# Kernel tuning notes

Measured on AMD Instinct MI355X. Metric: run time of the kernel, lower is better.

Reference implementation:

```python
import jax, jax.numpy as jnp
import numpy as np

B, N, Th, Td, Tw, Tp = 8, 3000, 24, 12, 24, 12
T2a, T2b, K = 64, 32, 3  # hidden temporal dims of the two STBlocks, Cheb order


def _laplacian(A):
    # PyG ChebConv with lambda_max=None -> lambda_max=2.0, sym normalization:
    # L_hat = 2L/lambda_max - I = -D^{-1/2} A D^{-1/2} with zero diagonal
    Aod = A * (1.0 - jnp.eye(A.shape[0], dtype=A.dtype))
    deg = Aod.sum(axis=1)
    dinv = jnp.where(deg > 0, deg ** -0.5, 0.0)
    return -(dinv[:, None] * Aod * dinv[None, :])


def _cheb(x, L, W, b):
    # Chebyshev graph conv, K=3. x: (B,N,Cin), L: (N,N), W: (K,Cin,Cout), b: (Cout,)
    Tx0 = x
    Tx1 = jnp.einsum('nm,bmi->bni', L, Tx0)
    Tx2 = 2.0 * jnp.einsum('nm,bmi->bni', L, Tx1) - Tx0
    out = (jnp.einsum('bni,io->bno', Tx0, W[0])
           + jnp.einsum('bni,io->bno', Tx1, W[1])
           + jnp.einsum('bni,io->bno', Tx2, W[2]))
    return out + b


def _tconv(x, w, b):
    # Conv1d(1, 1, 3, padding=1) over last axis. x: (B,N,T), w: (3,), b: scalar
    xp = jnp.pad(x, ((0, 0), (0, 0), (1, 1)))
    return w[0] * xp[..., :-2] + w[1] * xp[..., 1:-1] + w[2] * xp[..., 2:] + b


def _stblock(x, L, W, bg, cw, cb):
    x = jax.nn.relu(_cheb(x, L, W, bg))
    return jax.nn.relu(_tconv(x, cw, cb))


def _branch(X, L, W1, b1, c1w, c1b, W2, b2, c2w, c2b, WD, bD):
    x = X.reshape(X.shape[0], X.shape[1], X.shape[3])  # (B,N,T)
    x = _stblock(x, L, W1, b1, c1w, c1b)  # (B,N,64)
    x = _stblock(x, L, W2, b2, c2w, c2b)  # (B,N,32)
    return jax.nn.relu(x @ WD + bD)       # (B,N,Tp); forward only uses LinearD


def setup_inputs() -> dict:
    ks = jax.random.split(jax.random.key(0), 48)
    it = iter(range(48))

    def nrm(shape, s=1.0):
        return jax.random.normal(ks[next(it)], shape, jnp.float32) * s

    Xh = nrm((B, N, 1, Th))
    Xd = nrm((B, N, 1, Td))
    Xw = nrm((B, N, 1, Tw))
    u = jax.random.uniform(ks[next(it)], (N, N))
    w = jax.random.uniform(ks[next(it)], (N, N))
    A = jnp.where(u < 0.01, w, 0.0)
    A = 0.5 * (A + A.T)

    def gcn_p(ti, to):
        return nrm((K, ti, to), (2.0 / (ti + to)) ** 0.5), jnp.zeros((to,), jnp.float32)

    def conv_p():
        return nrm((K,), 0.4), nrm((), 0.1)

    Wh1, bh1 = gcn_p(Th, T2a); ch1w, ch1b = conv_p()
    Wh2, bh2 = gcn_p(T2a, T2b); ch2w, ch2b = conv_p()
    Wd1, bd1 = gcn_p(Td, T2a); cd1w, cd1b = conv_p()
    Wd2, bd2 = gcn_p(T2a, T2b); cd2w, cd2b = conv_p()
    Ww1, bw1 = gcn_p(Tw, T2a); cw1w, cw1b = conv_p()
    Ww2, bw2 = gcn_p(T2a, T2b); cw2w, cw2b = conv_p()
    WD = nrm((T2b, Tp), (2.0 / (T2b + Tp)) ** 0.5)
    bD = jnp.zeros((Tp,), jnp.float32)
    Fh = jax.random.uniform(ks[next(it)], (Tp,), jnp.float32)
    Fd = jax.random.uniform(ks[next(it)], (Tp,), jnp.float32)
    Fw = jax.random.uniform(ks[next(it)], (Tp,), jnp.float32)

    return dict(Xh=Xh, Xd=Xd, Xw=Xw, A=A,
                Wh1=Wh1, bh1=bh1, ch1w=ch1w, ch1b=ch1b, Wh2=Wh2, bh2=bh2, ch2w=ch2w, ch2b=ch2b,
                Wd1=Wd1, bd1=bd1, cd1w=cd1w, cd1b=cd1b, Wd2=Wd2, bd2=bd2, cd2w=cd2w, cd2b=cd2b,
                Ww1=Ww1, bw1=bw1, cw1w=cw1w, cw1b=cw1b, Ww2=Ww2, bw2=bw2, cw2w=cw2w, cw2b=cw2b,
                WD=WD, bD=bD, Fh=Fh, Fd=Fd, Fw=Fw)


def reference(Xh, Xd, Xw, A,
              Wh1, bh1, ch1w, ch1b, Wh2, bh2, ch2w, ch2b,
              Wd1, bd1, cd1w, cd1b, Wd2, bd2, cd2w, cd2b,
              Ww1, bw1, cw1w, cw1b, Ww2, bw2, cw2w, cw2b,
              WD, bD, Fh, Fd, Fw):
    L = _laplacian(A)
    Yh = _branch(Xh, L, Wh1, bh1, ch1w, ch1b, Wh2, bh2, ch2w, ch2b, WD, bD)
    Yd = _branch(Xd, L, Wd1, bd1, cd1w, cd1b, Wd2, bd2, cd2w, cd2b, WD, bD)
    Yw = _branch(Xw, L, Ww1, bw1, cw1w, cw1b, Ww2, bw2, cw2w, cw2b, WD, bD)
    Y = Fh * Yh + Fd * Yd + Fw * Yw  # Fusion: elementwise weighted sum over Tp
    return Y[:, :, None, :]  # (B,N,1,Tp)
```

## Files before the change

### kernel.cpp

```cpp
#include <hip/hip_runtime.h>

#define NN 3000
#define NB 8
#define TP 12
#define DMAX 128
#define F1T 480
#define F2T 768
#define Z1T 1536

struct BrW {
    const float *W1[3]; const float *b1[3]; const float *c1w[3]; const float *c1b[3];
    const float *W2[3]; const float *b2[3]; const float *c2w[3]; const float *c2b[3];
    const float *Fb[3];
};

__global__ void build_kernel(const float* __restrict__ A, int* __restrict__ colp,
                             float* __restrict__ valp, int* __restrict__ cnt,
                             float* __restrict__ dinv) {
    int n = blockIdx.x;
    int lane = threadIdx.x;
    const float* row = A + (size_t)n * NN;
    int base = 0;
    float s = 0.f;
    for (int start = 0; start < NN; start += 64) {
        int m = start + lane;
        float a = 0.f; bool nz = false;
        if (m < NN && m != n) {
            a = row[m];
            nz = (a != 0.f);
        }
        s += a;
        unsigned long long mask = __ballot(nz);
        int off = __popcll(mask & ((1ull << lane) - 1ull));
        if (nz) {
            int idx = base + off;
            if (idx < DMAX) { colp[n * DMAX + idx] = m; valp[n * DMAX + idx] = a; }
        }
        base += __popcll(mask);
    }
    for (int o = 32; o > 0; o >>= 1) s += __shfl_down(s, o);
    if (lane == 0) {
        cnt[n] = (base < DMAX) ? base : DMAX;
        dinv[n] = (s > 0.f) ? 1.0f / sqrtf(s) : 0.f;
    }
}

__global__ void scale_kernel(const int* __restrict__ colp, float* __restrict__ valp,
                             const int* __restrict__ cnt, const float* __restrict__ dinv) {
    int n = blockIdx.x;
    int j = threadIdx.x;
    if (j < cnt[n]) {
        int m = colp[n * DMAX + j];
        valp[n * DMAX + j] *= -dinv[n] * dinv[m];
    }
}

__global__ void pack_kernel(const float* __restrict__ Xh, const float* __restrict__ Xd,
                            const float* __restrict__ Xw, float* __restrict__ xcat) {
    int idx = blockIdx.x * blockDim.x + threadIdx.x;
    if (idx >= NN * F1T) return;
    int n = idx / F1T, r = idx % F1T;
    const float* src; int b, t, T;
    if (r < 192)      { src = Xh; T = 24; int rr = r;       b = rr / 24; t = rr % 24; }
    else if (r < 288) { src = Xd; T = 12; int rr = r - 192; b = rr / 12; t = rr % 12; }
    else              { src = Xw; T = 24; int rr = r - 288; b = rr / 24; t = rr % 24; }
    xcat[idx] = src[((size_t)b * NN + n) * T + t];
}

template <int F, int SLICE, int EPI>
__global__ void spmm_kernel(const int* __restrict__ colp, const float* __restrict__ valp,
                            const int* __restrict__ cnt, const float* __restrict__ x,
                            const float* __restrict__ aux, float* __restrict__ y) {
    int nwg = gridDim.x;
    int q = nwg >> 3;
    int bid = blockIdx.x;
    int w = (bid & 7) * q + (bid >> 3);
    int slice = w / NN;
    int n = w - slice * NN;
    int f = slice * SLICE + threadIdx.x;

    __shared__ int   scol[DMAX];
    __shared__ float sval[DMAX];
    int c = cnt[n];
    if (threadIdx.x < DMAX) {
        int j = threadIdx.x;
        bool ok = j < c;
        scol[j] = ok ? colp[n * DMAX + j] * F : 0;
        sval[j] = ok ? valp[n * DMAX + j] : 0.f;
    }
    __syncthreads();
    int c16 = (c + 15) & ~15;
    float a0 = 0.f, a1 = 0.f, a2 = 0.f, a3 = 0.f;
    float a4 = 0.f, a5 = 0.f, a6 = 0.f, a7 = 0.f;
    if (f < F) {
        for (int i = 0; i < c16; i += 16) {
            float g[16], w16[16];
            #pragma unroll
            for (int u = 0; u < 16; ++u) {
                int cc = scol[i + u];
                w16[u] = sval[i + u];
                g[u] = x[cc + f];
            }
            a0 += w16[0] * g[0];   a1 += w16[1] * g[1];
            a2 += w16[2] * g[2];   a3 += w16[3] * g[3];
            a4 += w16[4] * g[4];   a5 += w16[5] * g[5];
            a6 += w16[6] * g[6];   a7 += w16[7] * g[7];
            a0 += w16[8] * g[8];   a1 += w16[9] * g[9];
            a2 += w16[10] * g[10]; a3 += w16[11] * g[11];
            a4 += w16[12] * g[12]; a5 += w16[13] * g[13];
            a6 += w16[14] * g[14]; a7 += w16[15] * g[15];
        }
    }
    if (f >= F) return;
    float acc = ((a0 + a1) + (a2 + a3)) + ((a4 + a5) + (a6 + a7));
    size_t o = (size_t)n * F + f;
    if (EPI == 1) acc = 2.f * acc - aux[o];
    else if (EPI == 2) acc = aux[o] + 2.f * acc;
    y[o] = acc;
}

template <int T, int OFF, int BROFF>
__device__ __forceinline__ void combine1_body(
        int unit, const float* __restrict__ xcat, const float* __restrict__ t1cat,
        const float* __restrict__ t2cat, float* __restrict__ z1cat,
        const float* __restrict__ W, const float* __restrict__ bg,
        const float* __restrict__ cw, const float* __restrict__ cb, int co) {
    int n = unit / NB, b = unit % NB;
    size_t rowbase = (size_t)n * F1T + OFF + b * T;
    float xv0 = 0.f, xv1 = 0.f, xv2 = 0.f;
    if (co < T) {
        xv0 = xcat[rowbase + co];
        xv1 = t1cat[rowbase + co];
        xv2 = t2cat[rowbase + co];
    }
    float acc = bg[co];
    #pragma unroll
    for (int i = 0; i < T; ++i)
        acc += __shfl(xv0, i) * W[i * 64 + co];
    #pragma unroll
    for (int i = 0; i < T; ++i)
        acc += __shfl(xv1, i) * W[(T + i) * 64 + co];
    #pragma unroll
    for (int i = 0; i < T; ++i)
        acc += __shfl(xv2, i) * W[(2 * T + i) * 64 + co];
    float z = fmaxf(acc, 0.f);
    float left  = __shfl_up(z, 1);
    float right = __shfl_down(z, 1);
    if (co == 0) left = 0.f;
    if (co == 63) right = 0.f;
    float w0 = cw[0], w1 = cw[1], w2 = cw[2], bb = cb[0];
    float o = fmaxf(w0 * left + w1 * z + w2 * right + bb, 0.f);
    z1cat[(size_t)n * Z1T + BROFF + b * 64 + co] = o;
}

__global__ void combine1_all_kernel(const float* __restrict__ xcat,
                                    const float* __restrict__ t1cat,
                                    const float* __restrict__ t2cat,
                                    float* __restrict__ z1cat, BrW P) {
    int wid = threadIdx.x >> 6;
    int co = threadIdx.x & 63;
    int b = blockIdx.x;
    if (b < 6000) {
        int unit = b * 4 + wid;
        combine1_body<24, 0, 0>(unit, xcat, t1cat, t2cat, z1cat,
                                P.W1[0], P.b1[0], P.c1w[0], P.c1b[0], co);
    } else if (b < 12000) {
        int unit = (b - 6000) * 4 + wid;
        combine1_body<12, 192, 512>(unit, xcat, t1cat, t2cat, z1cat,
                                    P.W1[1], P.b1[1], P.c1w[1], P.c1b[1], co);
    } else {
        int unit = (b - 12000) * 4 + wid;
        combine1_body<24, 288, 1024>(unit, xcat, t1cat, t2cat, z1cat,
                                     P.W1[2], P.b1[2], P.c1w[2], P.c1b[2], co);
    }
}

#define GR 96
__global__ void __launch_bounds__(256, 2)
gemmy_kernel(const float* __restrict__ z1cat, float* __restrict__ y1cat,
             float* __restrict__ y2cat, float* __restrict__ c0cat, BrW P) {
    int tile = blockIdx.x;
    int br = blockIdx.y;
    __shared__ float sW[64 * 96];
    __shared__ float sZ[GR][65];
    const float* W = P.W2[br];
    for (int i = threadIdx.x; i < 6144; i += 256) {
        int k = i / 96, c = i % 96;
        int j = c / 3, m = c % 3;
        sW[i] = W[m * 2048 + k * 32 + j];
    }
    int row0 = tile * GR;
    for (int i = threadIdx.x; i < GR * 64; i += 256) {
        int r = i >> 6, k = i & 63;
        int rg = row0 + r;
        int n = rg >> 3, b = rg & 7;
        sZ[r][k] = z1cat[(size_t)n * Z1T + br * 512 + b * 64 + k];
    }
    __syncthreads();

    int rq = threadIdx.x >> 3;
    int g = threadIdx.x & 7;
    float acc[3][12];
    #pragma unroll
    for (int rr = 0; rr < 3; ++rr)
        #pragma unroll
        for (int j = 0; j < 12; ++j) acc[rr][j] = 0.f;

    #pragma unroll 4
    for (int k = 0; k < 64; ++k) {
        const float4* wr = reinterpret_cast<const float4*>(sW + k * 96 + g * 12);
        float4 wa = wr[0], wb = wr[1], wc = wr[2];
        #pragma unroll
        for (int rr = 0; rr < 3; ++rr) {
            float zv = sZ[rq * 3 + rr][k];
            acc[rr][0] += zv * wa.x; acc[rr][1] += zv * wa.y;
            acc[rr][2] += zv * wa.z; acc[rr][3] += zv * wa.w;
            acc[rr][4] += zv * wb.x; acc[rr][5] += zv * wb.y;
            acc[rr][6] += zv * wb.z; acc[rr][7] += zv * wb.w;
            acc[rr][8] += zv * wc.x; acc[rr][9] += zv * wc.y;
            acc[rr][10] += zv * wc.z; acc[rr][11] += zv * wc.w;
        }
    }

    const float* b2 = P.b2[br];
    float bj0 = b2[g * 4 + 0], bj1 = b2[g * 4 + 1], bj2 = b2[g * 4 + 2], bj3 = b2[g * 4 + 3];
    #pragma unroll
    for (int rr = 0; rr < 3; ++rr) {
        int rg = row0 + rq * 3 + rr;
        int n = rg >> 3, b = rg & 7;
        size_t obase = (size_t)n * F2T + br * 256 + b * 32;
        float bj[4] = {bj0, bj1, bj2, bj3};
        #pragma unroll
        for (int jj = 0; jj < 4; ++jj) {
            int j = g * 4 + jj;
            float a0 = acc[rr][jj * 3 + 0], a1 = acc[rr][jj * 3 + 1], a2 = acc[rr][jj * 3 + 2];
            y1cat[obase + j] = a1;
            y2cat[obase + j] = a2;
            c0cat[obase + j] = a0 - a2 + bj[jj];
        }
    }
}

__global__ void combine2_final_kernel(const float* __restrict__ c0cat,
                                      const float* __restrict__ vcat,
                                      const float* __restrict__ WD, const float* __restrict__ bD,
                                      float* __restrict__ out, BrW P) {
    int n = blockIdx.x;
    __shared__ float z2[3][NB][32];
    int unit = threadIdx.x >> 5;
    int co = threadIdx.x & 31;
    int br = unit >> 3, b = unit & 7;
    size_t o = (size_t)n * F2T + br * 256 + b * 32 + co;
    float a = fmaxf(c0cat[o] + vcat[o], 0.f);
    float left  = __shfl_up(a, 1);
    float right = __shfl_down(a, 1);
    if (co == 0) left = 0.f;
    if (co == 31) right = 0.f;
    float w0 = P.c2w[br][0], w1 = P.c2w[br][1], w2 = P.c2w[br][2], bb = P.c2b[br][0];
    z2[br][b][co] = fmaxf(w0 * left + w1 * a + w2 * right + bb, 0.f);
    __syncthreads();
    if (threadIdx.x < NB * TP) {
        int b2 = threadIdx.x / TP, tp = threadIdx.x % TP;
        float y = 0.f;
        for (int brr = 0; brr < 3; ++brr) {
            float s = bD[tp];
            const float* zz = z2[brr][b2];
            for (int c = 0; c < 32; ++c) s += zz[c] * WD[c * TP + tp];
            y += fmaxf(s, 0.f) * P.Fb[brr][tp];
        }
        out[((size_t)b2 * NN + n) * TP + tp] = y;
    }
}


static inline size_t align256(size_t x) { return (x + 255) & ~(size_t)255; }

extern "C" void kernel_launch(void* const* d_in, const int* in_sizes, int n_in,
                              void* d_out, int out_size, void* d_ws, size_t ws_size,
                              hipStream_t stream) {
    const float* Xh = (const float*)d_in[0];
    const float* Xd = (const float*)d_in[1];
    const float* Xw = (const float*)d_in[2];
    const float* A  = (const float*)d_in[3];
    const float* WD = (const float*)d_in[28];
    const float* bD = (const float*)d_in[29];

    BrW P;
    for (int br = 0; br < 3; ++br) {
        int base = 4 + br * 8;
        P.W1[br]  = (const float*)d_in[base + 0];
        P.b1[br]  = (const float*)d_in[base + 1];
        P.c1w[br] = (const float*)d_in[base + 2];
        P.c1b[br] = (const float*)d_in[base + 3];
        P.W2[br]  = (const float*)d_in[base + 4];
        P.b2[br]  = (const float*)d_in[base + 5];
        P.c2w[br] = (const float*)d_in[base + 6];
        P.c2b[br] = (const float*)d_in[base + 7];
        P.Fb[br]  = (const float*)d_in[30 + br];
    }

    char* p = (char*)d_ws;
    int*   colp  = (int*)p;   p += align256((size_t)NN * DMAX * 4);
    float* valp  = (float*)p; p += align256((size_t)NN * DMAX * 4);
    int*   cnt   = (int*)p;   p += align256(NN * 4);
    float* dinv  = (float*)p; p += align256(NN * 4);
    float* xcat  = (float*)p; p += align256((size_t)NN * F1T * 4);
    float* t1cat = (float*)p; p += align256((size_t)NN * F1T * 4);
    float* t2cat = (float*)p; p += align256((size_t)NN * F1T * 4);
    float* z1cat = (float*)p; p += align256((size_t)NN * Z1T * 4);
    float* y1cat = (float*)p; p += align256((size_t)NN * F2T * 4);
    float* y2cat = (float*)p; p += align256((size_t)NN * F2T * 4);
    float* c0cat = (float*)p; p += align256((size_t)NN * F2T * 4);
    float* scat  = (float*)p; p += align256((size_t)NN * F2T * 4);
    float* vcat  = (float*)p; p += align256((size_t)NN * F2T * 4);

    build_kernel<<<NN, 64, 0, stream>>>(A, colp, valp, cnt, dinv);
    scale_kernel<<<NN, DMAX, 0, stream>>>(colp, valp, cnt, dinv);
    pack_kernel<<<(NN * F1T + 255) / 256, 256, 0, stream>>>(Xh, Xd, Xw, xcat);

    spmm_kernel<F1T, 256, 0><<<6000, 256, 0, stream>>>(colp, valp, cnt, xcat, nullptr, t1cat);
    spmm_kernel<F1T, 256, 1><<<6000, 256, 0, stream>>>(colp, valp, cnt, t1cat, xcat, t2cat);
    combine1_all_kernel<<<18000, 256, 0, stream>>>(xcat, t1cat, t2cat, z1cat, P);

    gemmy_kernel<<<dim3(250, 3), 256, 0, stream>>>(z1cat, y1cat, y2cat, c0cat, P);
    spmm_kernel<F2T, 128, 2><<<18000, 128, 0, stream>>>(colp, valp, cnt, y2cat, y1cat, scat);
    spmm_kernel<F2T, 128, 0><<<18000, 128, 0, stream>>>(colp, valp, cnt, scat, nullptr, vcat);

    combine2_final_kernel<<<NN, 768, 0, stream>>>(c0cat, vcat, WD, bD, (float*)d_out, P);
}
```

Before: 201.6 us.

## Rewrite first-block Chebyshev combine as shared-memory tiled GEMM with register blocking

Replaces the per-wave shuffle-based dense combine (one wave per node-batch unit, weights read from global for every unit) with a tiled GEMM: each block stages the branch weight matrix and a 96-row tile of x/Tx1/Tx2 in shared memory, and each thread computes a 3x8 register tile. The temporal conv is applied across the 8-wide column groups with one shuffle at each edge, and results are stored as float4. This targets the redundant weight loads and the shuffle overhead of the old kernel. In exchange the grid drops to 750 blocks, which gives less parallelism and adds shared-memory staging and a block barrier.

After: 174.7 us. 13.4% less time.

```diff
diff --git a/kernel.cpp b/kernel.cpp
--- a/kernel.cpp
+++ b/kernel.cpp
@@ -120,58 +120,93 @@
 }
 
 template <int T, int OFF, int BROFF>
-__device__ __forceinline__ void combine1_body(
-        int unit, const float* __restrict__ xcat, const float* __restrict__ t1cat,
+__device__ __forceinline__ void combine1_gemm_body(
+        int tile, const float* __restrict__ xcat, const float* __restrict__ t1cat,
         const float* __restrict__ t2cat, float* __restrict__ z1cat,
         const float* __restrict__ W, const float* __restrict__ bg,
-        const float* __restrict__ cw, const float* __restrict__ cb, int co) {
-    int n = unit / NB, b = unit % NB;
-    size_t rowbase = (size_t)n * F1T + OFF + b * T;
-    float xv0 = 0.f, xv1 = 0.f, xv2 = 0.f;
-    if (co < T) {
-        xv0 = xcat[rowbase + co];
-        xv1 = t1cat[rowbase + co];
-        xv2 = t2cat[rowbase + co];
-    }
-    float acc = bg[co];
-    #pragma unroll
-    for (int i = 0; i < T; ++i)
-        acc += __shfl(xv0, i) * W[i * 64 + co];
-    #pragma unroll
-    for (int i = 0; i < T; ++i)
-        acc += __shfl(xv1, i) * W[(T + i) * 64 + co];
-    #pragma unroll
-    for (int i = 0; i < T; ++i)
-        acc += __shfl(xv2, i) * W[(2 * T + i) * 64 + co];
-    float z = fmaxf(acc, 0.f);
-    float left  = __shfl_up(z, 1);
-    float right = __shfl_down(z, 1);
-    if (co == 0) left = 0.f;
-    if (co == 63) right = 0.f;
+        const float* __restrict__ cw, const float* __restrict__ cb,
+        float* sW, float* sX) {
+    constexpr int K = 3 * T;
+    constexpr int LDA = K + 1;
+    int tid = threadIdx.x;
+    for (int i = tid; i < K * 64; i += 256) sW[i] = W[i];
+    int n0 = tile * 12;
+    #pragma unroll
+    for (int s = 0; s < 3; ++s) {
+        const float* src = (s == 0) ? xcat : (s == 1) ? t1cat : t2cat;
+        for (int i = tid; i < 96 * T; i += 256) {
+            int n_l = i / (8 * T), rem = i % (8 * T);
+            int b = rem / T, ii = rem % T;
+            float v = src[(size_t)(n0 + n_l) * F1T + OFF + b * T + ii];
+            sX[(n_l * 8 + b) * LDA + s * T + ii] = v;
+        }
+    }
+    __syncthreads();
+
+    int rq = tid >> 3;
+    int g  = tid & 7;
+    float acc[3][8];
+    #pragma unroll
+    for (int r = 0; r < 3; ++r)
+        #pragma unroll
+        for (int j = 0; j < 8; ++j) acc[r][j] = 0.f;
+
+    #pragma unroll 4
+    for (int k = 0; k < K; ++k) {
+        const float4* wr = reinterpret_cast<const float4*>(sW + k * 64 + g * 8);
+        float4 wa = wr[0], wb = wr[1];
+        #pragma unroll
+        for (int r = 0; r < 3; ++r) {
+            float zv = sX[(rq * 3 + r) * LDA + k];
+            acc[r][0] += zv * wa.x; acc[r][1] += zv * wa.y;
+            acc[r][2] += zv * wa.z; acc[r][3] += zv * wa.w;
+            acc[r][4] += zv * wb.x; acc[r][5] += zv * wb.y;
+            acc[r][6] += zv * wb.z; acc[r][7] += zv * wb.w;
+        }
+    }
+
+    float bgv[8];
+    #pragma unroll
+    for (int j = 0; j < 8; ++j) bgv[j] = bg[g * 8 + j];
     float w0 = cw[0], w1 = cw[1], w2 = cw[2], bb = cb[0];
-    float o = fmaxf(w0 * left + w1 * z + w2 * right + bb, 0.f);
-    z1cat[(size_t)n * Z1T + BROFF + b * 64 + co] = o;
-}
-
-__global__ void combine1_all_kernel(const float* __restrict__ xcat,
-                                    const float* __restrict__ t1cat,
-                                    const float* __restrict__ t2cat,
-                                    float* __restrict__ z1cat, BrW P) {
-    int wid = threadIdx.x >> 6;
-    int co = threadIdx.x & 63;
+
+    #pragma unroll
+    for (int r = 0; r < 3; ++r) {
+        float z[8];
+        #pragma unroll
+        for (int j = 0; j < 8; ++j) z[j] = fmaxf(acc[r][j] + bgv[j], 0.f);
+        float zl = __shfl_up(z[7], 1);
+        float zr = __shfl_down(z[0], 1);
+        float o[8];
+        #pragma unroll
+        for (int j = 0; j < 8; ++j) {
+            float left  = (j > 0) ? z[j - 1] : ((g > 0) ? zl : 0.f);
+            float right = (j < 7) ? z[j + 1] : ((g < 7) ? zr : 0.f);
+            o[j] = fmaxf(w0 * left + w1 * z[j] + w2 * right + bb, 0.f);
+        }
+        int unit = tile * 96 + rq * 3 + r;
+        int n = unit >> 3, b = unit & 7;
+        float* dst = z1cat + (size_t)n * Z1T + BROFF + b * 64 + g * 8;
+        reinterpret_cast<float4*>(dst)[0] = make_float4(o[0], o[1], o[2], o[3]);
+        reinterpret_cast<float4*>(dst)[1] = make_float4(o[4], o[5], o[6], o[7]);
+    }
+}
+
+__global__ void __launch_bounds__(256)
+combine1_all_kernel(const float* __restrict__ xcat, const float* __restrict__ t1cat,
+                    const float* __restrict__ t2cat, float* __restrict__ z1cat, BrW P) {
+    __shared__ float sW[72 * 64];
+    __shared__ float sX[96 * 73];
     int b = blockIdx.x;
-    if (b < 6000) {
-        int unit = b * 4 + wid;
-        combine1_body<24, 0, 0>(unit, xcat, t1cat, t2cat, z1cat,
-                                P.W1[0], P.b1[0], P.c1w[0], P.c1b[0], co);
-    } else if (b < 12000) {
-        int unit = (b - 6000) * 4 + wid;
-        combine1_body<12, 192, 512>(unit, xcat, t1cat, t2cat, z1cat,
-                                    P.W1[1], P.b1[1], P.c1w[1], P.c1b[1], co);
+    if (b < 250) {
+        combine1_gemm_body<24, 0, 0>(b, xcat, t1cat, t2cat, z1cat,
+                                     P.W1[0], P.b1[0], P.c1w[0], P.c1b[0], sW, sX);
+    } else if (b < 500) {
+        combine1_gemm_body<12, 192, 512>(b - 250, xcat, t1cat, t2cat, z1cat,
+                                         P.W1[1], P.b1[1], P.c1w[1], P.c1b[1], sW, sX);
     } else {
-        int unit = (b - 12000) * 4 + wid;
-        combine1_body<24, 288, 1024>(unit, xcat, t1cat, t2cat, z1cat,
-                                     P.W1[2], P.b1[2], P.c1w[2], P.c1b[2], co);
+        combine1_gemm_body<24, 288, 1024>(b - 500, xcat, t1cat, t2cat, z1cat,
+                                          P.W1[2], P.b1[2], P.c1w[2], P.c1b[2], sW, sX);
     }
 }
 
@@ -320,7 +355,7 @@
 
     spmm_kernel<F1T, 256, 0><<<6000, 256, 0, stream>>>(colp, valp, cnt, xcat, nullptr, t1cat);
     spmm_kernel<F1T, 256, 1><<<6000, 256, 0, stream>>>(colp, valp, cnt, t1cat, xcat, t2cat);
-    combine1_all_kernel<<<18000, 256, 0, stream>>>(xcat, t1cat, t2cat, z1cat, P);
+    combine1_all_kernel<<<750, 256, 0, stream>>>(xcat, t1cat, t2cat, z1cat, P);
 
     gemmy_kernel<<<dim3(250, 3), 256, 0, stream>>>(z1cat, y1cat, y2cat, c0cat, P);
     spmm_kernel<F2T, 128, 2><<<18000, 128, 0, stream>>>(colp, valp, cnt, y2cat, y1cat, scat);
```
